# Kernel optimization log

Hardware: AMD Instinct MI355X
Metric: run time of the kernel (lower is better)

The kernel has to match this reference:

```python
import jax, jax.numpy as jnp
import numpy as np

B, T, D, L, S, SPAN = 16, 8192, 256, 256, 128, 64


def setup_inputs() -> dict:
    key = jax.random.key(0)
    k1, k2, k3, k4 = jax.random.split(key, 4)
    word_reps = jax.random.normal(k1, (B, T, D), dtype=jnp.float32)
    # contiguous non-overlapping spans of length SPAN covering each doc
    starts = jnp.arange(S, dtype=jnp.int32) * SPAN            # [S]
    ends = starts + SPAN                                      # [S]
    offsets = jnp.broadcast_to(jnp.stack([starts, ends], -1), (B, S, 2))
    W1 = jax.random.normal(k2, (D, L), dtype=jnp.float32) * (1.0 / np.sqrt(D))
    b1 = jax.random.normal(k3, (L,), dtype=jnp.float32) * 0.01
    v = jax.random.normal(k4, (L,), dtype=jnp.float32) * (1.0 / np.sqrt(L))
    return {"word_reps": word_reps, "offsets": offsets, "W1": W1, "b1": b1, "v": v}


def reference(word_reps, offsets, W1, b1, v):
    # alpha = v(start(word_reps)) : two stacked linears, no activation -> [B,T]
    alpha = jnp.einsum("btl,l->bt", jnp.einsum("btd,dl->btl", word_reps, W1) + b1, v)

    starts = offsets[..., 0]                                  # [B,S]
    ends = offsets[..., 1]                                    # [B,S]
    pos = jnp.arange(word_reps.shape[1], dtype=offsets.dtype) # [T]
    mask = (pos[None, None, :] >= starts[..., None]) & (pos[None, None, :] < ends[..., None])  # [B,S,T]

    # ragged per-span softmax over token axis
    neg_inf = jnp.asarray(-jnp.inf, dtype=alpha.dtype)
    scores = jnp.where(mask, alpha[:, None, :], neg_inf)      # [B,S,T]
    s = jax.nn.softmax(scores, axis=-1)                       # [B,S,T]

    # attention-weighted sum pooling per span
    span_rep = jnp.einsum("bst,btd->bsd", s, word_reps)       # [B,S,D]

    # span lengths phi and last-token reps
    phi = (ends - starts).astype(word_reps.dtype)[..., None]  # [B,S,1]
    batch_idx = jnp.arange(word_reps.shape[0])[:, None]       # [B,1]
    span_ends = word_reps[batch_idx, ends - 1]                # [B,S,D]

    final_span_rep = jnp.concatenate([span_ends, span_rep, phi], axis=-1)  # [B,S,2D+1]
    prop_lens = jnp.full((word_reps.shape[0],), offsets.shape[1], dtype=jnp.int32)
    return final_span_rep, prop_lens
```

## Files before the change

kernel.cpp:

```cpp
#include <hip/hip_runtime.h>
#include <math.h>

#define B_   16
#define T_   8192
#define D_   256
#define L_   256
#define S_   128

__global__ __launch_bounds__(64) void prep_weff(const float* __restrict__ W1,
                                                const float* __restrict__ v,
                                                float* __restrict__ weff) {
    int d    = blockIdx.x;
    int lane = threadIdx.x;
    const float4* w4 = reinterpret_cast<const float4*>(W1 + (size_t)d * L_);
    const float4* v4 = reinterpret_cast<const float4*>(v);
    float4 a = w4[lane];
    float4 b = v4[lane];
    float s = a.x * b.x + a.y * b.y + a.z * b.z + a.w * b.w;
#pragma unroll
    for (int off = 32; off; off >>= 1) s += __shfl_xor(s, off);
    if (lane == 0) weff[d] = s;
}

__global__ __launch_bounds__(256) void span_kernel(const float* __restrict__ wr,
                                                   const int*   __restrict__ offsets,
                                                   const float* __restrict__ weff,
                                                   float*       __restrict__ out) {
    const int bs   = blockIdx.x;
    const int b    = bs >> 7;
    const int sp   = bs & (S_ - 1);
    const int tid  = threadIdx.x;
    const int wave = tid >> 6;
    const int lane = tid & 63;

    const int start = offsets[bs * 2 + 0];
    const int end   = offsets[bs * 2 + 1];
    const int len   = end - start;

    __shared__ float  alpha[64];
    __shared__ float4 part[4 * 64];

    const float4 we = reinterpret_cast<const float4*>(weff)[lane];

    float4 r[16];
    float  p[16];

#pragma unroll
    for (int i = 0; i < 16; ++i) {
        const int tok = wave + 4 * i;
        const int row_idx = b * T_ + ((start + tok < b * T_ + T_ - start) ? 0 : 0,
                              (start + tok));
        const int t_clamped = (tok < len) ? (start + tok) : (end - 1);
        const float4* row =
            reinterpret_cast<const float4*>(wr + (size_t)(b * T_ + t_clamped) * D_);
        float4 x = row[lane];
        r[i] = x;
        p[i] = x.x * we.x + x.y * we.y + x.z * we.z + x.w * we.w;
    }

#pragma unroll
    for (int i = 0; i < 16; ++i) {
        float t = p[i];
#pragma unroll
        for (int off = 32; off; off >>= 1) t += __shfl_xor(t, off);
        if (lane == 0) {
            const int tok = wave + 4 * i;
            alpha[tok] = (tok < len) ? t : -INFINITY;
        }
    }
    __syncthreads();

    const float a = alpha[lane];
    float m = a;
#pragma unroll
    for (int off = 32; off; off >>= 1) m = fmaxf(m, __shfl_xor(m, off));
    const float e = __expf(a - m);
    float ssum = e;
#pragma unroll
    for (int off = 32; off; off >>= 1) ssum += __shfl_xor(ssum, off);
    const float inv = 1.f / ssum;

    float4 acc = make_float4(0.f, 0.f, 0.f, 0.f);
#pragma unroll
    for (int i = 0; i < 16; ++i) {
        const float w = __shfl(e, wave + 4 * i);
        acc.x += w * r[i].x;
        acc.y += w * r[i].y;
        acc.z += w * r[i].z;
        acc.w += w * r[i].w;
    }
    part[wave * 64 + lane] = acc;
    __syncthreads();

    const size_t o = (size_t)bs * (2 * D_ + 1);
    if (wave == 0) {
        float4 t0 = part[lane];
        float4 t1 = part[64 + lane];
        float4 t2 = part[128 + lane];
        float4 t3 = part[192 + lane];
        out[o + D_ + lane * 4 + 0] = (t0.x + t1.x + t2.x + t3.x) * inv;
        out[o + D_ + lane * 4 + 1] = (t0.y + t1.y + t2.y + t3.y) * inv;
        out[o + D_ + lane * 4 + 2] = (t0.z + t1.z + t2.z + t3.z) * inv;
        out[o + D_ + lane * 4 + 3] = (t0.w + t1.w + t2.w + t3.w) * inv;
    } else if (wave == 1) {
        const float4* row =
            reinterpret_cast<const float4*>(wr + (size_t)(b * T_ + end - 1) * D_);
        float4 ee = row[lane];
        out[o + lane * 4 + 0] = ee.x;
        out[o + lane * 4 + 1] = ee.y;
        out[o + lane * 4 + 2] = ee.z;
        out[o + lane * 4 + 3] = ee.w;
    } else if (wave == 2 && lane == 0) {
        out[o + 2 * D_] = (float)len;
        if (sp == 0) out[(size_t)B_ * S_ * (2 * D_ + 1) + b] = (float)S_;
    }
}

extern "C" void kernel_launch(void* const* d_in, const int* in_sizes, int n_in,
                              void* d_out, int out_size, void* d_ws, size_t ws_size,
                              hipStream_t stream) {
    const float* word_reps = (const float*)d_in[0];
    const int*   offsets   = (const int*)d_in[1];
    const float* W1        = (const float*)d_in[2];
    const float* v         = (const float*)d_in[4];
    float*       out       = (float*)d_out;
    float*       weff      = (float*)d_ws;

    prep_weff<<<D_, 64, 0, stream>>>(W1, v, weff);
    span_kernel<<<B_ * S_, 256, 0, stream>>>(word_reps, offsets, weff, out);
}
```

Before: 34.03 us.

## Map one span per wavefront with streaming unnormalized softmax pooling

Each wavefront now handles a whole span, with four token groups of 16 lanes processing rows in parallel. Instead of storing all rows in registers and doing a max-subtracted softmax through shared memory, it accumulates exp(score)-weighted sums on the fly and reduces across groups with shuffles. This removes shared memory, __syncthreads and the per-token full-wave reductions, and cuts the grid by four. Dropping the max subtraction risks overflow in exp for large scores, and the grid now has fewer blocks to spread over the compute units.

```diff
diff --git a/kernel.cpp b/kernel.cpp
--- a/kernel.cpp
+++ b/kernel.cpp
@@ -26,91 +26,92 @@
                                                    const int*   __restrict__ offsets,
                                                    const float* __restrict__ weff,
                                                    float*       __restrict__ out) {
-    const int bs   = blockIdx.x;
-    const int b    = bs >> 7;
-    const int sp   = bs & (S_ - 1);
     const int tid  = threadIdx.x;
     const int wave = tid >> 6;
     const int lane = tid & 63;
+    const int bs   = blockIdx.x * 4 + wave;
+    const int b    = bs >> 7;
+    const int sp   = bs & (S_ - 1);
 
     const int start = offsets[bs * 2 + 0];
     const int end   = offsets[bs * 2 + 1];
     const int len   = end - start;
 
-    __shared__ float  alpha[64];
-    __shared__ float4 part[4 * 64];
+    const int g  = lane >> 4;
+    const int c0 = lane & 15;
 
-    const float4 we = reinterpret_cast<const float4*>(weff)[lane];
+    const float4* wf4 = reinterpret_cast<const float4*>(weff);
+    const float4 we0 = wf4[c0];
+    const float4 we1 = wf4[c0 + 16];
+    const float4 we2 = wf4[c0 + 32];
+    const float4 we3 = wf4[c0 + 48];
 
-    float4 r[16];
-    float  p[16];
+    float4 acc0 = make_float4(0.f, 0.f, 0.f, 0.f);
+    float4 acc1 = make_float4(0.f, 0.f, 0.f, 0.f);
+    float4 acc2 = make_float4(0.f, 0.f, 0.f, 0.f);
+    float4 acc3 = make_float4(0.f, 0.f, 0.f, 0.f);
+    float  z    = 0.f;
 
-#pragma unroll
-    for (int i = 0; i < 16; ++i) {
-        const int tok = wave + 4 * i;
-        const int row_idx = b * T_ + ((start + tok < b * T_ + T_ - start) ? 0 : 0,
-                              (start + tok));
-        const int t_clamped = (tok < len) ? (start + tok) : (end - 1);
-        const float4* row =
-            reinterpret_cast<const float4*>(wr + (size_t)(b * T_ + t_clamped) * D_);
-        float4 x = row[lane];
-        r[i] = x;
-        p[i] = x.x * we.x + x.y * we.y + x.z * we.z + x.w * we.w;
+    const float* base = wr + (size_t)(b * T_ + start) * D_;
+
+#pragma unroll 4
+    for (int p = 0; p < 16; ++p) {
+        const int t  = 4 * p + g;
+        const int tc = (t < len) ? t : (len - 1);
+        const float4* row = reinterpret_cast<const float4*>(base + (size_t)tc * D_);
+        float4 x0 = row[c0];
+        float4 x1 = row[c0 + 16];
+        float4 x2 = row[c0 + 32];
+        float4 x3 = row[c0 + 48];
+
+        float s = x0.x * we0.x + x0.y * we0.y + x0.z * we0.z + x0.w * we0.w
+                + x1.x * we1.x + x1.y * we1.y + x1.z * we1.z + x1.w * we1.w
+                + x2.x * we2.x + x2.y * we2.y + x2.z * we2.z + x2.w * we2.w
+                + x3.x * we3.x + x3.y * we3.y + x3.z * we3.z + x3.w * we3.w;
+        s += __shfl_xor(s, 1);
+        s += __shfl_xor(s, 2);
+        s += __shfl_xor(s, 4);
+        s += __shfl_xor(s, 8);
+
+        const float e = (t < len) ? __expf(s) : 0.f;
+        z += e;
+        acc0.x += e * x0.x; acc0.y += e * x0.y; acc0.z += e * x0.z; acc0.w += e * x0.w;
+        acc1.x += e * x1.x; acc1.y += e * x1.y; acc1.z += e * x1.z; acc1.w += e * x1.w;
+        acc2.x += e * x2.x; acc2.y += e * x2.y; acc2.z += e * x2.z; acc2.w += e * x2.w;
+        acc3.x += e * x3.x; acc3.y += e * x3.y; acc3.z += e * x3.z; acc3.w += e * x3.w;
     }
 
 #pragma unroll
-    for (int i = 0; i < 16; ++i) {
-        float t = p[i];
-#pragma unroll
-        for (int off = 32; off; off >>= 1) t += __shfl_xor(t, off);
-        if (lane == 0) {
-            const int tok = wave + 4 * i;
-            alpha[tok] = (tok < len) ? t : -INFINITY;
-        }
+    for (int off = 16; off <= 32; off <<= 1) {
+        z      += __shfl_xor(z, off);
+        acc0.x += __shfl_xor(acc0.x, off); acc0.y += __shfl_xor(acc0.y, off);
+        acc0.z += __shfl_xor(acc0.z, off); acc0.w += __shfl_xor(acc0.w, off);
+        acc1.x += __shfl_xor(acc1.x, off); acc1.y += __shfl_xor(acc1.y, off);
+        acc1.z += __shfl_xor(acc1.z, off); acc1.w += __shfl_xor(acc1.w, off);
+        acc2.x += __shfl_xor(acc2.x, off); acc2.y += __shfl_xor(acc2.y, off);
+        acc2.z += __shfl_xor(acc2.z, off); acc2.w += __shfl_xor(acc2.w, off);
+        acc3.x += __shfl_xor(acc3.x, off); acc3.y += __shfl_xor(acc3.y, off);
+        acc3.z += __shfl_xor(acc3.z, off); acc3.w += __shfl_xor(acc3.w, off);
     }
-    __syncthreads();
+    const float inv = 1.f / z;
 
-    const float a = alpha[lane];
-    float m = a;
-#pragma unroll
-    for (int off = 32; off; off >>= 1) m = fmaxf(m, __shfl_xor(m, off));
-    const float e = __expf(a - m);
-    float ssum = e;
-#pragma unroll
-    for (int off = 32; off; off >>= 1) ssum += __shfl_xor(ssum, off);
-    const float inv = 1.f / ssum;
-
-    float4 acc = make_float4(0.f, 0.f, 0.f, 0.f);
-#pragma unroll
-    for (int i = 0; i < 16; ++i) {
-        const float w = __shfl(e, wave + 4 * i);
-        acc.x += w * r[i].x;
-        acc.y += w * r[i].y;
-        acc.z += w * r[i].z;
-        acc.w += w * r[i].w;
-    }
-    part[wave * 64 + lane] = acc;
-    __syncthreads();
+    const float4 sel = (g == 0) ? acc0 : (g == 1) ? acc1 : (g == 2) ? acc2 : acc3;
 
     const size_t o = (size_t)bs * (2 * D_ + 1);
-    if (wave == 0) {
-        float4 t0 = part[lane];
-        float4 t1 = part[64 + lane];
-        float4 t2 = part[128 + lane];
-        float4 t3 = part[192 + lane];
-        out[o + D_ + lane * 4 + 0] = (t0.x + t1.x + t2.x + t3.x) * inv;
-        out[o + D_ + lane * 4 + 1] = (t0.y + t1.y + t2.y + t3.y) * inv;
-        out[o + D_ + lane * 4 + 2] = (t0.z + t1.z + t2.z + t3.z) * inv;
-        out[o + D_ + lane * 4 + 3] = (t0.w + t1.w + t2.w + t3.w) * inv;
-    } else if (wave == 1) {
-        const float4* row =
-            reinterpret_cast<const float4*>(wr + (size_t)(b * T_ + end - 1) * D_);
-        float4 ee = row[lane];
-        out[o + lane * 4 + 0] = ee.x;
-        out[o + lane * 4 + 1] = ee.y;
-        out[o + lane * 4 + 2] = ee.z;
-        out[o + lane * 4 + 3] = ee.w;
-    } else if (wave == 2 && lane == 0) {
+    out[o + D_ + lane * 4 + 0] = sel.x * inv;
+    out[o + D_ + lane * 4 + 1] = sel.y * inv;
+    out[o + D_ + lane * 4 + 2] = sel.z * inv;
+    out[o + D_ + lane * 4 + 3] = sel.w * inv;
+
+    const float4* lrow =
+        reinterpret_cast<const float4*>(wr + (size_t)(b * T_ + end - 1) * D_);
+    const float4 le = lrow[lane];
+    out[o + lane * 4 + 0] = le.x;
+    out[o + lane * 4 + 1] = le.y;
+    out[o + lane * 4 + 2] = le.z;
+    out[o + lane * 4 + 3] = le.w;
+
+    if (lane == 0) {
         out[o + 2 * D_] = (float)len;
         if (sp == 0) out[(size_t)B_ * S_ * (2 * D_ + 1) + b] = (float)S_;
     }
@@ -127,5 +128,5 @@
     float*       weff      = (float*)d_ws;
 
     prep_weff<<<D_, 64, 0, stream>>>(W1, v, weff);
-    span_kernel<<<B_ * S_, 256, 0, stream>>>(word_reps, offsets, weff, out);
+    span_kernel<<<(B_ * S_) / 4, 256, 0, stream>>>(word_reps, offsets, weff, out);
 }
```

After: 33.97 us. No clear change (-0.2%).
